# Kernel optimization log

Hardware: AMD Instinct MI355X
Metric: run time of the kernel (lower is better)

Reference implementation:

```python
import jax, jax.numpy as jnp
import numpy as np

N_NODES = 100000
N_EDGES = 1600000
NODES_PER_GRAPH = 100  # equal-sized graphs -> batch = arange // 100
POOL_K = 30


def setup_inputs() -> dict:
    key = jax.random.key(0)
    ks = jax.random.split(key, 8)
    F_IN, H1, H2, OUT = 128, 128, 128, 64
    x = jax.random.normal(ks[0], (N_NODES, F_IN), dtype=jnp.float32)
    edge_index = jax.random.randint(ks[1], (2, N_EDGES), 0, N_NODES, dtype=jnp.int64)
    batch = (jnp.arange(N_NODES, dtype=jnp.int64) // NODES_PER_GRAPH)
    # Glorot-ish init for weights, zero bias (as PyG GCNConv defaults)
    W1 = jax.random.normal(ks[2], (F_IN, H1), dtype=jnp.float32) / np.sqrt(F_IN)
    b1 = jnp.zeros((H1,), dtype=jnp.float32)
    W2 = jax.random.normal(ks[3], (H1, H2), dtype=jnp.float32) / np.sqrt(H1)
    b2 = jnp.zeros((H2,), dtype=jnp.float32)
    W3 = jax.random.normal(ks[4], (H2, OUT), dtype=jnp.float32) / np.sqrt(H2)
    b3 = jnp.zeros((OUT,), dtype=jnp.float32)
    return {"x": x, "edge_index": edge_index, "batch": batch,
            "W1": W1, "b1": b1, "W2": W2, "b2": b2, "W3": W3, "b3": b3}


def _gcn_conv(x, src, dst, W, b):
    """PyG GCNConv: xW, add self-loops, symmetric D^-1/2 A D^-1/2 scatter-add, +bias."""
    n = x.shape[0]
    loops = jnp.arange(n, dtype=src.dtype)
    row = jnp.concatenate([src, loops])  # message source
    col = jnp.concatenate([dst, loops])  # aggregation target
    xw = x @ W
    deg = jax.ops.segment_sum(jnp.ones(col.shape[0], x.dtype), col, num_segments=n)
    dinv = jnp.where(deg > 0, jax.lax.rsqrt(deg), 0.0)
    norm = dinv[row] * dinv[col]  # [E+N]
    out = jax.ops.segment_sum(xw[row] * norm[:, None], col, num_segments=n)
    return out + b


def _sort_pool(x, k):
    """global_sort_pool: per-graph descending sort by last channel, take top-k, flatten.
    Graphs are equal-sized and contiguous, so reshape to [B, P, C]."""
    n, c = x.shape
    xb = x.reshape(n // NODES_PER_GRAPH, NODES_PER_GRAPH, c)  # [B, P, C]
    order = jnp.argsort(-xb[..., -1], axis=1)[:, :k]          # [B, k]
    topk = jnp.take_along_axis(xb, order[..., None], axis=1)  # [B, k, C]
    return topk.reshape(topk.shape[0], k * c)


def reference(x, edge_index, batch, W1, b1, W2, b2, W3, b3):
    src, dst = edge_index[0], edge_index[1]
    h = jax.nn.relu(_gcn_conv(x, src, dst, W1, b1))
    h = jax.nn.relu(_gcn_conv(h, src, dst, W2, b2))
    h = _gcn_conv(h, src, dst, W3, b3)
    return _sort_pool(h, POOL_K)
```

## Files before the change

### kernel.cpp

```cpp
#include <hip/hip_runtime.h>
#include <math.h>

static inline size_t ws_align(size_t x) { return (x + 255) & ~(size_t)255; }

__global__ void count_kernel(const int* __restrict__ dst, int* __restrict__ counts, int E) {
  int e = blockIdx.x * 256 + threadIdx.x;
  if (e < E) atomicAdd(&counts[dst[e]], 1);
}

__global__ __launch_bounds__(256) void scanA_kernel(const int* __restrict__ counts,
    int* __restrict__ bsums, int n) {
  __shared__ int red[4];
  const int base = blockIdx.x * 1024;
  const int tid = threadIdx.x;
  int s = 0;
  #pragma unroll
  for (int u = 0; u < 4; ++u) {
    int i = base + u * 256 + tid;
    s += (i < n) ? counts[i] : 0;
  }
  #pragma unroll
  for (int m = 1; m < 64; m <<= 1) s += __shfl_xor(s, m, 64);
  if ((tid & 63) == 0) red[tid >> 6] = s;
  __syncthreads();
  if (tid == 0) bsums[blockIdx.x] = red[0] + red[1] + red[2] + red[3];
}

__global__ __launch_bounds__(128) void scanB_kernel(int* __restrict__ bsums, int nb) {
  __shared__ int tmp[129];
  int tid = threadIdx.x;
  tmp[tid] = (tid < nb) ? bsums[tid] : 0;
  __syncthreads();
  if (tid == 0) {
    int run = 0;
    for (int i = 0; i < nb; ++i) { int v = tmp[i]; tmp[i] = run; run += v; }
  }
  __syncthreads();
  if (tid < nb) bsums[tid] = tmp[tid];
}

__global__ __launch_bounds__(1024) void scanC_kernel(const int* __restrict__ counts,
    const int* __restrict__ bsums, int* __restrict__ offsets, int* __restrict__ cursor,
    double* __restrict__ dinv, int n) {
  __shared__ int warpsums[16];
  const int tid = threadIdx.x;
  const int lane = tid & 63, wid = tid >> 6;
  const int i = blockIdx.x * 1024 + tid;
  int v = (i < n) ? counts[i] : 0;
  int x = v;
  #pragma unroll
  for (int d = 1; d < 64; d <<= 1) {
    int y = __shfl_up(x, d, 64);
    if (lane >= d) x += y;
  }
  if (lane == 63) warpsums[wid] = x;
  __syncthreads();
  if (wid == 0) {
    int w = (lane < 16) ? warpsums[lane] : 0;
    #pragma unroll
    for (int d = 1; d < 16; d <<= 1) {
      int y = __shfl_up(w, d, 64);
      if (lane >= d) w += y;
    }
    if (lane < 16) warpsums[lane] = w;
  }
  __syncthreads();
  int excl = bsums[blockIdx.x] + x - v + (wid > 0 ? warpsums[wid - 1] : 0);
  if (i < n) {
    offsets[i] = excl;
    cursor[i] = excl;
    dinv[i] = 1.0 / sqrt((double)(v + 1));
    if (i == n - 1) offsets[n] = excl + v;
  }
}

__global__ void scatter_kernel(const int* __restrict__ src, const int* __restrict__ dst,
    int* __restrict__ cursor, int* __restrict__ srcs, double* __restrict__ ew,
    const double* __restrict__ dinv, int E, int use_ew) {
  int e = blockIdx.x * 256 + threadIdx.x;
  if (e < E) {
    int s = src[e], d = dst[e];
    int p = atomicAdd(&cursor[d], 1);
    srcs[p] = s;
    if (use_ew) ew[p] = dinv[s] * dinv[d];
  }
}

__global__ void cvtW_kernel(const float* __restrict__ W1, const float* __restrict__ W2,
    const float* __restrict__ W3, double* __restrict__ W1d, double* __restrict__ W2d,
    double* __restrict__ W3d) {
  int i = blockIdx.x * 256 + threadIdx.x;
  if (i < 16384) { W1d[i] = (double)W1[i]; W2d[i] = (double)W2[i]; }
  if (i < 8192)  { W3d[i] = (double)W3[i]; }
}

template<int H>
__global__ __launch_bounds__(256) void gemm_kernel(const float* __restrict__ X,
    const double* __restrict__ Wd, float* __restrict__ out, int N) {
  __shared__ float xs[128][68];
  const int tid  = threadIdx.x;
  const int row0 = blockIdx.x * 64;
  #pragma unroll
  for (int p = 0; p < 8; ++p) {
    int idx = p * 256 + tid;
    int r = idx >> 5;
    int c4 = idx & 31;
    int grow = row0 + r;
    float4 v = make_float4(0.f, 0.f, 0.f, 0.f);
    if (grow < N) v = *(const float4*)(X + (size_t)grow * 128 + c4 * 4);
    xs[c4 * 4 + 0][r] = v.x;
    xs[c4 * 4 + 1][r] = v.y;
    xs[c4 * 4 + 2][r] = v.z;
    xs[c4 * 4 + 3][r] = v.w;
  }
  __syncthreads();
  constexpr int CPT = H / 16;
  const int rowg = tid & 15;
  const int colg = tid >> 4;
  double acc[4][CPT];
  #pragma unroll
  for (int j = 0; j < 4; ++j)
    #pragma unroll
    for (int h = 0; h < CPT; ++h) acc[j][h] = 0.0;

  #pragma unroll 2
  for (int k = 0; k < 128; k += 2) {
    float4 av0 = *(const float4*)(&xs[k][rowg * 4]);
    float4 av1 = *(const float4*)(&xs[k + 1][rowg * 4]);
    double a0[4], a1[4];
    a0[0] = (double)av0.x; a0[1] = (double)av0.y; a0[2] = (double)av0.z; a0[3] = (double)av0.w;
    a1[0] = (double)av1.x; a1[1] = (double)av1.y; a1[2] = (double)av1.z; a1[3] = (double)av1.w;
    double b0[CPT], b1[CPT];
    const double* w0 = Wd + (size_t)k * H + colg * CPT;
    const double* w1 = w0 + H;
    #pragma unroll
    for (int q = 0; q < CPT / 2; ++q) {
      double2 v0 = *(const double2*)(w0 + q * 2);
      double2 v1 = *(const double2*)(w1 + q * 2);
      b0[q*2+0] = v0.x; b0[q*2+1] = v0.y;
      b1[q*2+0] = v1.x; b1[q*2+1] = v1.y;
    }
    #pragma unroll
    for (int j = 0; j < 4; ++j)
      #pragma unroll
      for (int h = 0; h < CPT; ++h) {
        acc[j][h] = fma(a0[j], b0[h], acc[j][h]);
        acc[j][h] = fma(a1[j], b1[h], acc[j][h]);
      }
  }
  #pragma unroll
  for (int j = 0; j < 4; ++j) {
    int grow = row0 + rowg * 4 + j;
    if (grow < N) {
      float* o = out + (size_t)grow * H + colg * CPT;
      #pragma unroll
      for (int q = 0; q < CPT / 4; ++q) {
        float4 v = make_float4((float)acc[j][q*4+0], (float)acc[j][q*4+1],
                               (float)acc[j][q*4+2], (float)acc[j][q*4+3]);
        *(float4*)(o + q * 4) = v;
      }
    }
  }
}

template<int C, bool RELU, bool USE_EW>
__global__ __launch_bounds__(256) void gather_kernel(const float* __restrict__ xw,
    const double* __restrict__ dinv, const int* __restrict__ offs,
    const int* __restrict__ srcs, const double* __restrict__ ew,
    const float* __restrict__ bias, float* __restrict__ out, int N) {
  constexpr int LPR = C / 4;
  constexpr int EPI = 64 / LPR;
  constexpr int U = 8;
  const int node = blockIdx.x * 4 + (threadIdx.x >> 6);
  if (node >= N) return;
  const int lane = threadIdx.x & 63;
  const int grp  = lane / LPR;
  const int c0   = (lane % LPR) * 4;
  const int e0 = offs[node], e1 = offs[node + 1];
  const double di = dinv[node];
  double a0 = 0.0, a1 = 0.0, a2 = 0.0, a3 = 0.0;

  for (int base = e0; base < e1; base += U * EPI) {
    int ss[U];
    double ww[U];
    float4 vv[U];
    #pragma unroll
    for (int u = 0; u < U; ++u) {
      int ee = base + u * EPI + grp;
      int cl = ee < e1 ? ee : e1 - 1;
      ss[u] = srcs[cl];
      if (USE_EW) ww[u] = ew[cl];
    }
    #pragma unroll
    for (int u = 0; u < U; ++u) {
      vv[u] = *(const float4*)(xw + (size_t)ss[u] * C + c0);
      if (!USE_EW) ww[u] = dinv[ss[u]];
    }
    #pragma unroll
    for (int u = 0; u < U; ++u) {
      int ee = base + u * EPI + grp;
      double w = (ee < e1) ? ww[u] : 0.0;
      a0 = fma(w, (double)vv[u].x, a0);
      a1 = fma(w, (double)vv[u].y, a1);
      a2 = fma(w, (double)vv[u].z, a2);
      a3 = fma(w, (double)vv[u].w, a3);
    }
  }
  #pragma unroll
  for (int m = LPR; m < 64; m <<= 1) {
    a0 += __shfl_xor(a0, m, 64);
    a1 += __shfl_xor(a1, m, 64);
    a2 += __shfl_xor(a2, m, 64);
    a3 += __shfl_xor(a3, m, 64);
  }
  if (grp == 0) {
    const double d2 = di * di;
    float4 sv = *(const float4*)(xw + (size_t)node * C + c0);
    float4 bv = *(const float4*)(bias + c0);
    double o0, o1, o2, o3;
    if (USE_EW) {
      o0 = a0 + fma(d2, (double)sv.x, (double)bv.x);
      o1 = a1 + fma(d2, (double)sv.y, (double)bv.y);
      o2 = a2 + fma(d2, (double)sv.z, (double)bv.z);
      o3 = a3 + fma(d2, (double)sv.w, (double)bv.w);
    } else {
      o0 = fma(di, a0, fma(d2, (double)sv.x, (double)bv.x));
      o1 = fma(di, a1, fma(d2, (double)sv.y, (double)bv.y));
      o2 = fma(di, a2, fma(d2, (double)sv.z, (double)bv.z));
      o3 = fma(di, a3, fma(d2, (double)sv.w, (double)bv.w));
    }
    if (RELU) {
      o0 = o0 > 0.0 ? o0 : 0.0; o1 = o1 > 0.0 ? o1 : 0.0;
      o2 = o2 > 0.0 ? o2 : 0.0; o3 = o3 > 0.0 ? o3 : 0.0;
    }
    *(float4*)(out + (size_t)node * C + c0) =
        make_float4((float)o0, (float)o1, (float)o2, (float)o3);
  }
}

__global__ __launch_bounds__(128) void sortpool_kernel(const float* __restrict__ h,
    float* __restrict__ out) {
  __shared__ float sv[128];
  __shared__ int si[128];
  int g = blockIdx.x;
  int tid = threadIdx.x;
  const float* hg = h + (size_t)g * 100 * 64;
  if (tid < 100) {
    sv[tid] = hg[tid * 64 + 63];
    si[tid] = tid;
  } else {
    sv[tid] = -3.0e38f;
    si[tid] = 1 << 30;
  }
  __syncthreads();
  for (int k = 2; k <= 128; k <<= 1) {
    for (int j = k >> 1; j > 0; j >>= 1) {
      int i = tid;
      int l = i ^ j;
      if (l > i) {
        float va = sv[i], vb = sv[l];
        int ia = si[i], ib = si[l];
        bool a_before_b = (va > vb) || (va == vb && ia < ib);
        bool up = ((i & k) == 0);
        bool sw = up ? !a_before_b : a_before_b;
        if (sw) { sv[i] = vb; sv[l] = va; si[i] = ib; si[l] = ia; }
      }
      __syncthreads();
    }
  }
  for (int t = tid; t < 30 * 64; t += 128) {
    int kk = t >> 6;
    int c = t & 63;
    out[(size_t)g * (30 * 64) + t] = hg[si[kk] * 64 + c];
  }
}

extern "C" void kernel_launch(void* const* d_in, const int* in_sizes, int n_in,
                              void* d_out, int out_size, void* d_ws, size_t ws_size,
                              hipStream_t stream) {
  const float* x  = (const float*)d_in[0];
  const int*   ei = (const int*)d_in[1];
  const float* W1 = (const float*)d_in[3];
  const float* b1 = (const float*)d_in[4];
  const float* W2 = (const float*)d_in[5];
  const float* b2 = (const float*)d_in[6];
  const float* W3 = (const float*)d_in[7];
  const float* b3 = (const float*)d_in[8];

  const int N = in_sizes[0] / 128;
  const int E = in_sizes[1] / 2;
  const int* src = ei;
  const int* dst = ei + E;
  (void)n_in; (void)out_size;

  const int nb = (N + 1023) / 1024;

  char* ws = (char*)d_ws;
  size_t off = 0;
  auto alloc = [&](size_t bytes) { char* p = ws + off; off = ws_align(off + bytes); return p; };
  float*  xw      = (float*) alloc((size_t)N * 128 * 4);
  float*  h       = (float*) alloc((size_t)N * 128 * 4);
  double* dinv    = (double*)alloc((size_t)N * 8);
  int*    offsets = (int*)   alloc(((size_t)N + 1) * 4);
  int*    cursor  = (int*)   alloc((size_t)N * 4);
  int*    counts  = (int*)   alloc((size_t)N * 4);
  int*    srcs    = (int*)   alloc((size_t)E * 4);
  double* W1d     = (double*)alloc(16384 * 8);
  double* W2d     = (double*)alloc(16384 * 8);
  double* W3d     = (double*)alloc(8192 * 8);
  int*    bsums   = (int*)   alloc((size_t)(nb + 1) * 4);
  double* ew      = (double*)alloc((size_t)E * 8);
  const bool use_ew = (off <= ws_size);

  hipMemsetAsync(counts, 0, (size_t)N * 4, stream);
  count_kernel<<<(E + 255) / 256, 256, 0, stream>>>(dst, counts, E);
  scanA_kernel<<<nb, 256, 0, stream>>>(counts, bsums, N);
  scanB_kernel<<<1, 128, 0, stream>>>(bsums, nb);
  scanC_kernel<<<nb, 1024, 0, stream>>>(counts, bsums, offsets, cursor, dinv, N);
  scatter_kernel<<<(E + 255) / 256, 256, 0, stream>>>(src, dst, cursor, srcs, ew, dinv, E, use_ew ? 1 : 0);
  cvtW_kernel<<<64, 256, 0, stream>>>(W1, W2, W3, W1d, W2d, W3d);

  const int gblocks  = (N + 63) / 64;
  const int nblocks4 = (N + 3) / 4;

  gemm_kernel<128><<<gblocks, 256, 0, stream>>>(x, W1d, xw, N);
  if (use_ew) {
    gather_kernel<128, true,  true><<<nblocks4, 256, 0, stream>>>(xw, dinv, offsets, srcs, ew, b1, h, N);
    gemm_kernel<128><<<gblocks, 256, 0, stream>>>(h, W2d, xw, N);
    gather_kernel<128, true,  true><<<nblocks4, 256, 0, stream>>>(xw, dinv, offsets, srcs, ew, b2, h, N);
    gemm_kernel<64 ><<<gblocks, 256, 0, stream>>>(h, W3d, xw, N);
    gather_kernel<64,  false, true><<<nblocks4, 256, 0, stream>>>(xw, dinv, offsets, srcs, ew, b3, h, N);
  } else {
    gather_kernel<128, true,  false><<<nblocks4, 256, 0, stream>>>(xw, dinv, offsets, srcs, ew, b1, h, N);
    gemm_kernel<128><<<gblocks, 256, 0, stream>>>(h, W2d, xw, N);
    gather_kernel<128, true,  false><<<nblocks4, 256, 0, stream>>>(xw, dinv, offsets, srcs, ew, b2, h, N);
    gemm_kernel<64 ><<<gblocks, 256, 0, stream>>>(h, W3d, xw, N);
    gather_kernel<64,  false, false><<<nblocks4, 256, 0, stream>>>(xw, dinv, offsets, srcs, ew, b3, h, N);
  }
  sortpool_kernel<<<N / 100, 128, 0, stream>>>(h, (float*)d_out);
}
```

Measured before the change: 885.4 us.

## Double-buffer FP64 GEMM operands, swizzle LDS layout, store edge weights as float

The GEMM's shared-memory tile is rewritten with an XOR swizzle in place of row padding. The k-loop now software-pipelines the next A (LDS) and B (global weight) loads ahead of the FMAs, and launch bounds are raised to request more waves per SIMD. Separately, the per-edge normalization weights are stored as float instead of double, halving that gather stream. Risks are register spills under the tighter launch bounds, and a small precision loss in the edge weights.

```diff
diff --git a/kernel.cpp b/kernel.cpp
--- a/kernel.cpp
+++ b/kernel.cpp
@@ -75,14 +75,14 @@
 }
 
 __global__ void scatter_kernel(const int* __restrict__ src, const int* __restrict__ dst,
-    int* __restrict__ cursor, int* __restrict__ srcs, double* __restrict__ ew,
+    int* __restrict__ cursor, int* __restrict__ srcs, float* __restrict__ ew,
     const double* __restrict__ dinv, int E, int use_ew) {
   int e = blockIdx.x * 256 + threadIdx.x;
   if (e < E) {
     int s = src[e], d = dst[e];
     int p = atomicAdd(&cursor[d], 1);
     srcs[p] = s;
-    if (use_ew) ew[p] = dinv[s] * dinv[d];
+    if (use_ew) ew[p] = (float)(dinv[s] * dinv[d]);
   }
 }
 
@@ -94,59 +94,86 @@
   if (i < 8192)  { W3d[i] = (double)W3[i]; }
 }
 
-template<int H>
-__global__ __launch_bounds__(256) void gemm_kernel(const float* __restrict__ X,
+template<int H, int MINW>
+__global__ __launch_bounds__(256, MINW) void gemm_kernel(const float* __restrict__ X,
     const double* __restrict__ Wd, float* __restrict__ out, int N) {
-  __shared__ float xs[128][68];
+  __shared__ float xs[128 * 64];
   const int tid  = threadIdx.x;
   const int row0 = blockIdx.x * 64;
   #pragma unroll
   for (int p = 0; p < 8; ++p) {
     int idx = p * 256 + tid;
-    int r = idx >> 5;
+    int r  = idx >> 5;
     int c4 = idx & 31;
     int grow = row0 + r;
     float4 v = make_float4(0.f, 0.f, 0.f, 0.f);
     if (grow < N) v = *(const float4*)(X + (size_t)grow * 128 + c4 * 4);
-    xs[c4 * 4 + 0][r] = v.x;
-    xs[c4 * 4 + 1][r] = v.y;
-    xs[c4 * 4 + 2][r] = v.z;
-    xs[c4 * 4 + 3][r] = v.w;
+    const int g = r >> 2, s = r & 3;
+    float vals[4] = {v.x, v.y, v.z, v.w};
+    #pragma unroll
+    for (int j = 0; j < 4; ++j) {
+      int k = c4 * 4 + j;
+      xs[k * 64 + ((g ^ (k & 15)) << 2) + s] = vals[j];
+    }
   }
   __syncthreads();
   constexpr int CPT = H / 16;
   const int rowg = tid & 15;
   const int colg = tid >> 4;
+  const float4* xsv = (const float4*)xs;
+  const double* wbase = Wd + colg * CPT;
+
   double acc[4][CPT];
   #pragma unroll
   for (int j = 0; j < 4; ++j)
     #pragma unroll
     for (int h = 0; h < CPT; ++h) acc[j][h] = 0.0;
 
-  #pragma unroll 2
+  float4 aA = xsv[(0 << 4) + (rowg ^ 0)];
+  float4 aB;
+  double bA[CPT], bB[CPT];
+  #pragma unroll
+  for (int q = 0; q < CPT / 2; ++q) {
+    double2 t = *(const double2*)(wbase + 0 * H + q * 2);
+    bA[2*q] = t.x; bA[2*q+1] = t.y;
+  }
+
+  #pragma unroll 1
   for (int k = 0; k < 128; k += 2) {
-    float4 av0 = *(const float4*)(&xs[k][rowg * 4]);
-    float4 av1 = *(const float4*)(&xs[k + 1][rowg * 4]);
-    double a0[4], a1[4];
-    a0[0] = (double)av0.x; a0[1] = (double)av0.y; a0[2] = (double)av0.z; a0[3] = (double)av0.w;
-    a1[0] = (double)av1.x; a1[1] = (double)av1.y; a1[2] = (double)av1.z; a1[3] = (double)av1.w;
-    double b0[CPT], b1[CPT];
-    const double* w0 = Wd + (size_t)k * H + colg * CPT;
-    const double* w1 = w0 + H;
+    aB = xsv[((k + 1) << 4) + (rowg ^ ((k + 1) & 15))];
     #pragma unroll
     for (int q = 0; q < CPT / 2; ++q) {
-      double2 v0 = *(const double2*)(w0 + q * 2);
-      double2 v1 = *(const double2*)(w1 + q * 2);
-      b0[q*2+0] = v0.x; b0[q*2+1] = v0.y;
-      b1[q*2+0] = v1.x; b1[q*2+1] = v1.y;
-    }
-    #pragma unroll
-    for (int j = 0; j < 4; ++j)
+      double2 t = *(const double2*)(wbase + (size_t)(k + 1) * H + q * 2);
+      bB[2*q] = t.x; bB[2*q+1] = t.y;
+    }
+    {
+      double a0 = (double)aA.x, a1 = (double)aA.y, a2 = (double)aA.z, a3 = (double)aA.w;
       #pragma unroll
       for (int h = 0; h < CPT; ++h) {
-        acc[j][h] = fma(a0[j], b0[h], acc[j][h]);
-        acc[j][h] = fma(a1[j], b1[h], acc[j][h]);
-      }
+        acc[0][h] = fma(a0, bA[h], acc[0][h]);
+        acc[1][h] = fma(a1, bA[h], acc[1][h]);
+        acc[2][h] = fma(a2, bA[h], acc[2][h]);
+        acc[3][h] = fma(a3, bA[h], acc[3][h]);
+      }
+    }
+    if (k + 2 < 128) {
+      aA = xsv[((k + 2) << 4) + (rowg ^ ((k + 2) & 15))];
+      #pragma unroll
+      for (int q = 0; q < CPT / 2; ++q) {
+        double2 t = *(const double2*)(wbase + (size_t)(k + 2) * H + q * 2);
+        bA[2*q] = t.x; bA[2*q+1] = t.y;
+      }
+    }
+    {
+      double a0 = (double)aB.x, a1 = (double)aB.y, a2 = (double)aB.z, a3 = (double)aB.w;
+      #pragma unroll
+      for (int h = 0; h < CPT; ++h) {
+        acc[0][h] = fma(a0, bB[h], acc[0][h]);
+        acc[1][h] = fma(a1, bB[h], acc[1][h]);
+        acc[2][h] = fma(a2, bB[h], acc[2][h]);
+        acc[3][h] = fma(a3, bB[h], acc[3][h]);
+      }
+    }
   }
   #pragma unroll
   for (int j = 0; j < 4; ++j) {
@@ -166,7 +193,7 @@
 template<int C, bool RELU, bool USE_EW>
 __global__ __launch_bounds__(256) void gather_kernel(const float* __restrict__ xw,
     const double* __restrict__ dinv, const int* __restrict__ offs,
-    const int* __restrict__ srcs, const double* __restrict__ ew,
+    const int* __restrict__ srcs, const float* __restrict__ ew,
     const float* __restrict__ bias, float* __restrict__ out, int N) {
   constexpr int LPR = C / 4;
   constexpr int EPI = 64 / LPR;
@@ -189,7 +216,7 @@
       int ee = base + u * EPI + grp;
       int cl = ee < e1 ? ee : e1 - 1;
       ss[u] = srcs[cl];
-      if (USE_EW) ww[u] = ew[cl];
+      if (USE_EW) ww[u] = (double)ew[cl];
     }
     #pragma unroll
     for (int u = 0; u < U; ++u) {
@@ -309,7 +336,7 @@
   double* W2d     = (double*)alloc(16384 * 8);
   double* W3d     = (double*)alloc(8192 * 8);
   int*    bsums   = (int*)   alloc((size_t)(nb + 1) * 4);
-  double* ew      = (double*)alloc((size_t)E * 8);
+  float*  ew      = (float*) alloc((size_t)E * 4);
   const bool use_ew = (off <= ws_size);
 
   hipMemsetAsync(counts, 0, (size_t)N * 4, stream);
@@ -323,18 +350,18 @@
   const int gblocks  = (N + 63) / 64;
   const int nblocks4 = (N + 3) / 4;
 
-  gemm_kernel<128><<<gblocks, 256, 0, stream>>>(x, W1d, xw, N);
+  gemm_kernel<128, 3><<<gblocks, 256, 0, stream>>>(x, W1d, xw, N);
   if (use_ew) {
     gather_kernel<128, true,  true><<<nblocks4, 256, 0, stream>>>(xw, dinv, offsets, srcs, ew, b1, h, N);
-    gemm_kernel<128><<<gblocks, 256, 0, stream>>>(h, W2d, xw, N);
+    gemm_kernel<128, 3><<<gblocks, 256, 0, stream>>>(h, W2d, xw, N);
     gather_kernel<128, true,  true><<<nblocks4, 256, 0, stream>>>(xw, dinv, offsets, srcs, ew, b2, h, N);
-    gemm_kernel<64 ><<<gblocks, 256, 0, stream>>>(h, W3d, xw, N);
+    gemm_kernel<64, 4><<<gblocks, 256, 0, stream>>>(h, W3d, xw, N);
     gather_kernel<64,  false, true><<<nblocks4, 256, 0, stream>>>(xw, dinv, offsets, srcs, ew, b3, h, N);
   } else {
     gather_kernel<128, true,  false><<<nblocks4, 256, 0, stream>>>(xw, dinv, offsets, srcs, ew, b1, h, N);
-    gemm_kernel<128><<<gblocks, 256, 0, stream>>>(h, W2d, xw, N);
+    gemm_kernel<128, 3><<<gblocks, 256, 0, stream>>>(h, W2d, xw, N);
     gather_kernel<128, true,  false><<<nblocks4, 256, 0, stream>>>(xw, dinv, offsets, srcs, ew, b2, h, N);
-    gemm_kernel<64 ><<<gblocks, 256, 0, stream>>>(h, W3d, xw, N);
+    gemm_kernel<64, 4><<<gblocks, 256, 0, stream>>>(h, W3d, xw, N);
     gather_kernel<64,  false, false><<<nblocks4, 256, 0, stream>>>(xw, dinv, offsets, srcs, ew, b3, h, N);
   }
   sortpool_kernel<<<N / 100, 128, 0, stream>>>(h, (float*)d_out);
```

After: 878.6 us. No clear change (-0.8%).
